# Performance work log

Measured on AMD Instinct MI355X. Metric: run time of the kernel, lower is better.

Reference implementation:

```python
import jax, jax.numpy as jnp
import numpy as np

N, D, K = 4096, 1024, 32
MARGIN = 0.3
OP_TYPE = "weighty"


def setup_inputs() -> dict:
    key = jax.random.key(0)
    k1, k2, k3, k4, k5 = jax.random.split(key, 5)
    return {
        "inputs": jax.random.normal(k1, (N, D), jnp.float32),
        "prediction": jax.random.normal(k2, (N, K), jnp.float32),
        "targets": jax.random.randint(k3, (N,), 0, K),
        "true_targets": jax.random.randint(k4, (N,), 0, K),
        "prob": jax.random.uniform(k5, (N,), jnp.float32),
        "threshold": jnp.float32(0.5),
    }


def _weighty(d1, d2, pair_type, op_type):
    # vectorized translation of weighty_new
    if op_type == "mean":
        return (d1 + d2) / 2.0
    if op_type == "max":
        return jnp.maximum(d1, d2)
    if op_type == "min":
        return jnp.minimum(d1, d2)
    if op_type == "max-min":
        return jnp.maximum(d1, d2) if pair_type == 1 else jnp.minimum(d1, d2)
    # op_type == 'weighty'
    if pair_type == 1:
        e1, e2 = jnp.exp(d1), jnp.exp(d2)
        return (e1 * d1 + e2 * d2) / (e1 + e2)
    e1, e2 = jnp.exp(-d1), jnp.exp(-d2)
    return (e1 * d1 + e2 * d2) / (e1 + e2 + 1e-6)


def reference(inputs, prediction, targets, true_targets, prob, threshold):
    n = inputs.shape[0]
    rows = jnp.arange(n)
    # pairwise euclidean dist (GEMM-based, matches addmm_ formulation)
    sq = jnp.sum(inputs * inputs, axis=1)
    dist = sq[:, None] + sq[None, :] - 2.0 * (inputs @ inputs.T)
    dist = jnp.sqrt(jnp.clip(dist, 1e-12, None))  # [n, n]

    same = targets[:, None] == targets[None, :]
    conf = prob >= threshold

    # negatives sorted ascending by dist; positives sorted descending by dist
    neg_order = jnp.argsort(jnp.where(~same, dist, jnp.inf), axis=1)   # [n,n]
    pos_order = jnp.argsort(jnp.where(same, -dist, jnp.inf), axis=1)   # [n,n]
    hp = pos_order[:, 0]   # hardest positive (max dist)
    hn = neg_order[:, 0]   # hardest negative (min dist)
    d_ap = dist[rows, hp]
    d_an = dist[rows, hn]

    cp = prob[hp] >= threshold
    cn = prob[hn] >= threshold
    fn = jnp.argmax(prediction, axis=1)[hn] == targets  # hard neg is a false negative

    # neg re-selection: ranks 1..10 first with prob>=t, else rank 11 (loop_cnt cap 10)
    neg_cand = neg_order[:, 1:12]                       # [n,11]
    ok_n = prob[neg_cand] >= threshold
    sel_n = jnp.where(ok_n[:, :10].any(axis=1), jnp.argmax(ok_n[:, :10], axis=1), 10)
    d_nn = dist[rows, neg_cand[rows, sel_n]]

    # pos re-selection: descending ranks 1..5 first with prob>=t, else rank 6 (loop_cnt cap 5)
    pos_cand = pos_order[:, 1:7]                        # [n,6]
    ok_p = prob[pos_cand] >= threshold
    sel_p = jnp.where(ok_p[:, :5].any(axis=1), jnp.argmax(ok_p[:, :5], axis=1), 5)
    d_np = dist[rows, pos_cand[rows, sel_p]]

    w1 = _weighty(d_ap, d_an, 1, OP_TYPE)
    w0 = _weighty(d_ap, d_an, 0, OP_TYPE)

    case_b = cp & (~cn) & fn                 # confident pos, unconfident FN neg
    case_cd = (~cp) & (cn | (~fn))           # unconfident pos branches that re-select pos
    inv = (~cp) & (~cn) & fn                 # inverse loss branch

    ap = jnp.where(case_b, w1, jnp.where(case_cd, d_np, d_ap))
    an = jnp.where(case_b, d_nn, jnp.where(case_cd, w0, d_an))

    per = jnp.where(inv,
                    jax.nn.relu(an - ap + MARGIN),
                    jax.nn.relu(ap - an + MARGIN))
    conff = conf.astype(per.dtype)
    cnt = jnp.sum(conf.astype(jnp.int32))
    loss = jnp.where(cnt > 0, jnp.sum(per * conff) / jnp.maximum(cnt, 1).astype(per.dtype), 0.0)
    correct = jnp.sum(((an >= ap) & conf).astype(jnp.int32))
    return loss, correct, cnt
```

## Files before the change

### kernel.cpp

```cpp
#include <hip/hip_runtime.h>
#include <hip/hip_bf16.h>
#include <stdint.h>

typedef _Float16 half8 __attribute__((ext_vector_type(8)));
typedef _Float16 half4 __attribute__((ext_vector_type(4)));
typedef float f32x4 __attribute__((ext_vector_type(4)));
typedef unsigned long long u64;

#define N_ROWS 4096
#define DIM 1024
#define KCLS 32
#define MARGIN_F 0.3f
#define SENTN 0xFFFFFFFFFFFFFFFFull

typedef const __attribute__((address_space(1))) void GASV;
typedef __attribute__((address_space(3))) void LASV;

__device__ __forceinline__ void gload_lds16(const void* g, void* l) {
    __builtin_amdgcn_global_load_lds((GASV*)g, (LASV*)l, 16, 0, 0);
}

__global__ __launch_bounds__(256) void prep_kernel(
    const float* __restrict__ inputs, const float* __restrict__ prediction,
    _Float16* __restrict__ xh, float* __restrict__ sq, int* __restrict__ pred_cls)
{
    int wid = threadIdx.x >> 6, lane = threadIdx.x & 63;
    int r = blockIdx.x * 4 + wid;
    const float* row = inputs + (size_t)r * DIM;
    _Float16* hrow = xh + (size_t)r * DIM;
    float s = 0.f;
#pragma unroll
    for (int c = 0; c < 4; ++c) {
        int idx = lane * 4 + c * 256;
        float4 v = *(const float4*)(row + idx);
        s += v.x * v.x + v.y * v.y + v.z * v.z + v.w * v.w;
        half4 h;
        h.x = (_Float16)v.x; h.y = (_Float16)v.y;
        h.z = (_Float16)v.z; h.w = (_Float16)v.w;
        *(half4*)(hrow + idx) = h;
    }
#pragma unroll
    for (int off = 32; off; off >>= 1) s += __shfl_xor(s, off);

    u64 key = 0ull;
    if (lane < KCLS) {
        unsigned b = __float_as_uint(prediction[(size_t)r * KCLS + lane]);
        unsigned u = (b & 0x80000000u) ? ~b : (b | 0x80000000u);
        key = ((u64)u << 32) | (unsigned)(KCLS - 1 - lane);
    }
#pragma unroll
    for (int off = 32; off; off >>= 1) {
        u64 o = __shfl_xor(key, off);
        if (o > key) key = o;
    }
    if (lane == 0) {
        sq[r] = s;
        pred_cls[r] = KCLS - 1 - (int)(key & 0xFFFFFFFFu);
    }
}

__global__ __launch_bounds__(512) void gemm_kernel(
    const _Float16* __restrict__ X, const float* __restrict__ sq,
    const int* __restrict__ targets,
    float* __restrict__ out, int mode, int rb0)
{
    __shared__ __align__(16) _Float16 As[128 * 64];
    __shared__ __align__(16) _Float16 Bs[128 * 64];
    int tid = threadIdx.x;

    int bx, by;
    bool diag = false, mirror = false;
    if (mode == 0) {
        int u = ((int)blockIdx.x & 7) * 66 + ((int)blockIdx.x >> 3);
        int t_ = (int)((sqrtf(8.f * u + 1.f) - 1.f) * 0.5f);
        while ((t_ + 1) * (t_ + 2) / 2 <= u) ++t_;
        while (t_ * (t_ + 1) / 2 > u) --t_;
        by = t_;
        bx = u - t_ * (t_ + 1) / 2;
        diag = (bx == by);
        mirror = !diag;
    } else {
        int nwg = gridDim.x;
        int q = nwg >> 3;
        int swz = ((int)blockIdx.x & 7) * q + ((int)blockIdx.x >> 3);
        int nbx = nwg / 32;
        bx = swz % nbx;
        by = swz / nbx;
    }

    int rs = tid >> 3;
    int ss = tid & 7;
    int srcslot = ss ^ (rs & 7);
    const _Float16* gA = X + (size_t)(rb0 + bx * 128 + rs) * DIM + srcslot * 8;
    const _Float16* gB = X + (size_t)(by * 128 + rs) * DIM + srcslot * 8;
    _Float16* lA = As + tid * 8;
    _Float16* lB = Bs + tid * 8;

    int wid = tid >> 6, lane = tid & 63;
    int wr = (wid >> 2) * 64, wc = (wid & 3) * 32;
    int fr = lane & 15, q4 = lane >> 4;

    f32x4 acc[4][2];
#pragma unroll
    for (int m = 0; m < 4; ++m)
#pragma unroll
        for (int n = 0; n < 2; ++n) acc[m][n] = (f32x4){0.f, 0.f, 0.f, 0.f};

    for (int k0 = 0; k0 < DIM; k0 += 64) {
#pragma unroll
        for (int p = 0; p < 2; ++p) {
            gload_lds16(gA + k0 + (size_t)(p * 64) * DIM, lA + p * 4096);
            if (!diag) gload_lds16(gB + k0 + (size_t)(p * 64) * DIM, lB + p * 4096);
        }
        __syncthreads();
        const _Float16* Bsrc = diag ? As : Bs;
#pragma unroll
        for (int ks = 0; ks < 2; ++ks) {
            half8 a[4], b[2];
#pragma unroll
            for (int m = 0; m < 4; ++m) {
                int row = wr + m * 16 + fr;
                int s = (ks * 4 + q4) ^ (row & 7);
                a[m] = *(const half8*)(As + row * 64 + s * 8);
            }
#pragma unroll
            for (int n = 0; n < 2; ++n) {
                int brow = wc + n * 16 + fr;
                int s = (ks * 4 + q4) ^ (brow & 7);
                b[n] = *(const half8*)(Bsrc + brow * 64 + s * 8);
            }
#pragma unroll
            for (int m = 0; m < 4; ++m)
#pragma unroll
                for (int n = 0; n < 2; ++n)
                    acc[m][n] = __builtin_amdgcn_mfma_f32_16x16x32_f16(a[m], b[n], acc[m][n], 0, 0, 0);
        }
        __syncthreads();
    }

    int rbase = rb0 + bx * 128 + wr + q4 * 4;
    float sqr_[4][4];
    int trr[4][4];
#pragma unroll
    for (int m = 0; m < 4; ++m)
#pragma unroll
        for (int q = 0; q < 4; ++q) {
            sqr_[m][q] = sq[rbase + m * 16 + q];
            trr[m][q] = targets[rbase + m * 16 + q];
        }

#pragma unroll
    for (int n = 0; n < 2; ++n) {
        int col = by * 128 + wc + n * 16 + fr;
        float sqc = sq[col];
        int tc = targets[col];
#pragma unroll
        for (int m = 0; m < 4; ++m) {
            int row0 = rbase + m * 16;
            float4 d;
            unsigned u0, u1, u2, u3;
            u0 = __float_as_uint(fmaxf(sqr_[m][0] + sqc - 2.f * acc[m][n][0], 1e-12f));
            u1 = __float_as_uint(fmaxf(sqr_[m][1] + sqc - 2.f * acc[m][n][1], 1e-12f));
            u2 = __float_as_uint(fmaxf(sqr_[m][2] + sqc - 2.f * acc[m][n][2], 1e-12f));
            u3 = __float_as_uint(fmaxf(sqr_[m][3] + sqc - 2.f * acc[m][n][3], 1e-12f));
            d.x = __uint_as_float((u0 & ~1u) | (unsigned)(trr[m][0] == tc));
            d.y = __uint_as_float((u1 & ~1u) | (unsigned)(trr[m][1] == tc));
            d.z = __uint_as_float((u2 & ~1u) | (unsigned)(trr[m][2] == tc));
            d.w = __uint_as_float((u3 & ~1u) | (unsigned)(trr[m][3] == tc));
            out[(size_t)(row0 + 0) * N_ROWS + col] = d.x;
            out[(size_t)(row0 + 1) * N_ROWS + col] = d.y;
            out[(size_t)(row0 + 2) * N_ROWS + col] = d.z;
            out[(size_t)(row0 + 3) * N_ROWS + col] = d.w;
            if (mirror)
                *(float4*)&out[(size_t)col * N_ROWS + row0] = d;
        }
    }
}

__global__ __launch_bounds__(256) void select_kernel(
    const float* __restrict__ dot,
    const int* __restrict__ targets, const float* __restrict__ prob,
    const int* __restrict__ pred_cls, const float* __restrict__ thr_p,
    int rb0, float* __restrict__ per_term, int* __restrict__ corr_flag)
{
    __shared__ unsigned Tn[4], Tp[4];
    __shared__ u64 negCand[64];
    __shared__ u64 posCand[64];
    __shared__ unsigned cnts[2];
    __shared__ u64 sN[12], sP[7];
    __shared__ u64 red[4];
    __shared__ u64 bcast;

    int t = threadIdx.x, lane = t & 63, w = t >> 6;
    int rloc = blockIdx.x, r = rb0 + rloc;
    const float* drow = dot + (size_t)rloc * N_ROWS;

    if (t < 64) { negCand[t] = SENTN; posCand[t] = 0ull; }
    if (t < 2) cnts[t] = 0u;

    unsigned bits[16];
    unsigned mneg = 0xFFFFFFFFu, mpos = 0u;
#pragma unroll
    for (int q = 0; q < 4; ++q) {
        int col0 = q * 1024 + t * 4;
        float4 dv = *(const float4*)(drow + col0);
        int j = q * 4;
        unsigned b;
        b = __float_as_uint(dv.x); bits[j + 0] = b;
        if (b & 1u) mpos = mpos > b ? mpos : b; else mneg = mneg < b ? mneg : b;
        b = __float_as_uint(dv.y); bits[j + 1] = b;
        if (b & 1u) mpos = mpos > b ? mpos : b; else mneg = mneg < b ? mneg : b;
        b = __float_as_uint(dv.z); bits[j + 2] = b;
        if (b & 1u) mpos = mpos > b ? mpos : b; else mneg = mneg < b ? mneg : b;
        b = __float_as_uint(dv.w); bits[j + 3] = b;
        if (b & 1u) mpos = mpos > b ? mpos : b; else mneg = mneg < b ? mneg : b;
    }

    unsigned T3 = 0xFFFFFFFFu, m = mneg;
#pragma unroll
    for (int rd = 0; rd < 3; ++rd) {
        unsigned b = m;
#pragma unroll
        for (int off = 32; off; off >>= 1) {
            unsigned o = __shfl_xor(b, off);
            b = o < b ? o : b;
        }
        T3 = b;
        if (m == b) m = 0xFFFFFFFFu;
    }
    unsigned P2 = 0u, mp = mpos;
#pragma unroll
    for (int rd = 0; rd < 2; ++rd) {
        unsigned b = mp;
#pragma unroll
        for (int off = 32; off; off >>= 1) {
            unsigned o = __shfl_xor(b, off);
            b = o > b ? o : b;
        }
        P2 = b;
        if (mp == b) mp = 0u;
    }
    if (lane == 0) { Tn[w] = T3; Tp[w] = P2; }
    __syncthreads();

    unsigned TnB = Tn[0];
    TnB = Tn[1] > TnB ? Tn[1] : TnB;
    TnB = Tn[2] > TnB ? Tn[2] : TnB;
    TnB = Tn[3] > TnB ? Tn[3] : TnB;
    unsigned TpB = Tp[0];
    TpB = Tp[1] < TpB ? Tp[1] : TpB;
    TpB = Tp[2] < TpB ? Tp[2] : TpB;
    TpB = Tp[3] < TpB ? Tp[3] : TpB;

#pragma unroll
    for (int q = 0; q < 4; ++q) {
#pragma unroll
        for (int e = 0; e < 4; ++e) {
            int j = q * 4 + e;
            int col = q * 1024 + t * 4 + e;
            unsigned b = bits[j];
            if (!(b & 1u) && b <= TnB) {
                unsigned s = atomicAdd(&cnts[0], 1u);
                if (s < 64u) negCand[s] = ((u64)b << 32) | (unsigned)col;
            }
            if ((b & 1u) && b >= TpB) {
                unsigned s = atomicAdd(&cnts[1], 1u);
                if (s < 64u) posCand[s] = ((u64)b << 32) | (unsigned)(N_ROWS - 1 - col);
            }
        }
    }
    __syncthreads();

    bool fb = (cnts[0] > 64u) || (cnts[1] > 64u);

    if (!fb) {
        if (w == 0) {
            u64 v = negCand[lane];
#pragma unroll
            for (int k = 2; k <= 64; k <<= 1) {
#pragma unroll
                for (int j = 32; j; j >>= 1) {
                    if (j >= k) continue;
                    u64 o = __shfl_xor(v, j);
                    bool up = (lane & k) == 0;
                    bool small = (lane & j) == 0;
                    bool keepmin = (small == up);
                    u64 lo = v < o ? v : o, hi = v < o ? o : v;
                    v = keepmin ? lo : hi;
                }
            }
            if (lane < 12) sN[lane] = v;
        } else if (w == 1) {
            u64 v = ~posCand[lane];
#pragma unroll
            for (int k = 2; k <= 64; k <<= 1) {
#pragma unroll
                for (int j = 32; j; j >>= 1) {
                    if (j >= k) continue;
                    u64 o = __shfl_xor(v, j);
                    bool up = (lane & k) == 0;
                    bool small = (lane & j) == 0;
                    bool keepmin = (small == up);
                    u64 lo = v < o ? v : o, hi = v < o ? o : v;
                    v = keepmin ? lo : hi;
                }
            }
            if (lane < 7) sP[lane] = ~v;
        }
    } else {
        unsigned remN = 0, remP = 0;
        for (int rd = 0; rd < 12; ++rd) {
            u64 best = SENTN;
#pragma unroll
            for (int q = 0; q < 4; ++q)
#pragma unroll
                for (int e = 0; e < 4; ++e) {
                    int j = q * 4 + e;
                    int col = q * 1024 + t * 4 + e;
                    bool valid = !(bits[j] & 1u) && !((remN >> j) & 1u);
                    u64 nk = valid ? (((u64)bits[j] << 32) | (unsigned)col) : SENTN;
                    best = nk < best ? nk : best;
                }
#pragma unroll
            for (int off = 32; off; off >>= 1) {
                u64 o = __shfl_xor(best, off);
                best = o < best ? o : best;
            }
            if (lane == 0) red[w] = best;
            __syncthreads();
            if (t == 0) {
                u64 b0 = red[0];
                b0 = red[1] < b0 ? red[1] : b0;
                b0 = red[2] < b0 ? red[2] : b0;
                b0 = red[3] < b0 ? red[3] : b0;
                sN[rd] = b0; bcast = b0;
            }
            __syncthreads();
            u64 b0 = bcast;
#pragma unroll
            for (int q = 0; q < 4; ++q)
#pragma unroll
                for (int e = 0; e < 4; ++e) {
                    int j = q * 4 + e;
                    int col = q * 1024 + t * 4 + e;
                    if ((((u64)bits[j] << 32) | (unsigned)col) == b0) remN |= 1u << j;
                }
            __syncthreads();
        }
        for (int rd = 0; rd < 7; ++rd) {
            u64 best = 0ull;
#pragma unroll
            for (int q = 0; q < 4; ++q)
#pragma unroll
                for (int e = 0; e < 4; ++e) {
                    int j = q * 4 + e;
                    int col = q * 1024 + t * 4 + e;
                    bool valid = (bits[j] & 1u) && !((remP >> j) & 1u);
                    u64 pk = valid ? (((u64)bits[j] << 32) | (unsigned)(N_ROWS - 1 - col)) : 0ull;
                    best = pk > best ? pk : best;
                }
#pragma unroll
            for (int off = 32; off; off >>= 1) {
                u64 o = __shfl_xor(best, off);
                best = o > best ? o : best;
            }
            if (lane == 0) red[w] = best;
            __syncthreads();
            if (t == 0) {
                u64 b0 = red[0];
                b0 = red[1] > b0 ? red[1] : b0;
                b0 = red[2] > b0 ? red[2] : b0;
                b0 = red[3] > b0 ? red[3] : b0;
                sP[rd] = b0; bcast = b0;
            }
            __syncthreads();
            u64 b0 = bcast;
#pragma unroll
            for (int q = 0; q < 4; ++q)
#pragma unroll
                for (int e = 0; e < 4; ++e) {
                    int j = q * 4 + e;
                    int col = q * 1024 + t * 4 + e;
                    if ((((u64)bits[j] << 32) | (unsigned)(N_ROWS - 1 - col)) == b0) remP |= 1u << j;
                }
            __syncthreads();
        }
    }
    __syncthreads();

    if (w == 0) {
        float thr = *thr_p;
        int tr = targets[r];
        u64 kN = (lane < 12) ? sN[lane] : SENTN;
        u64 kP = (lane >= 32 && lane < 39) ? sP[lane - 32] : 0ull;
        int idxN = ((int)(kN & 0xFFFFFFFFull)) & (N_ROWS - 1);
        int idxP = (N_ROWS - 1 - (int)(kP & 0xFFFFFFFFull)) & (N_ROWS - 1);
        bool confN = (lane < 12) && kN != SENTN && (prob[idxN] >= thr);
        bool confP = (lane >= 32 && lane < 39) && kP != 0ull && (prob[idxP] >= thr);
        u64 balN = __ballot(confN);
        u64 balP = __ballot(confP);

        u64 mN_ = balN & 0x7FEull;
        int selN = mN_ ? (__ffsll(mN_) - 1) : 11;
        unsigned dnn_bits = __shfl((unsigned)(kN >> 32), selN);
        u64 mP_ = balP & (0x3Eull << 32);
        int selP = mP_ ? (__ffsll(mP_) - 1) : 38;
        unsigned dnp_bits = __shfl((unsigned)(kP >> 32), selP);
        unsigned dap_bits = __shfl((unsigned)(kP >> 32), 32);

        if (lane == 0) {
            float d_ap = sqrtf(__uint_as_float(dap_bits));
            float d_an = sqrtf(__uint_as_float((unsigned)(kN >> 32)));
            int hn = idxN;
            bool cp = (balP >> 32) & 1ull;
            bool cn = balN & 1ull;
            bool fn = (pred_cls[hn] == tr);
            float d_nn = sqrtf(__uint_as_float(dnn_bits));
            float d_np = sqrtf(__uint_as_float(dnp_bits));

            float e1p = __expf(d_ap), e2p = __expf(d_an);
            float w1 = (e1p * d_ap + e2p * d_an) / (e1p + e2p);
            float e1n = __expf(-d_ap), e2n = __expf(-d_an);
            float w0 = (e1n * d_ap + e2n * d_an) / (e1n + e2n + 1e-6f);
            bool case_b = cp && !cn && fn;
            bool case_cd = !cp && (cn || !fn);
            bool inv = !cp && !cn && fn;
            float ap = case_b ? w1 : (case_cd ? d_np : d_ap);
            float an = case_b ? d_nn : (case_cd ? w0 : d_an);
            float per = inv ? fmaxf(an - ap + MARGIN_F, 0.f)
                            : fmaxf(ap - an + MARGIN_F, 0.f);
            per_term[r] = per;
            corr_flag[r] = (an >= ap) ? 1 : 0;
        }
    }
}

__global__ __launch_bounds__(256) void finalize_kernel(
    const float* __restrict__ per_term, const int* __restrict__ corr_flag,
    const float* __restrict__ prob, const float* __restrict__ thr_p,
    float* __restrict__ out)
{
    __shared__ float sred[4]; __shared__ int cred[4]; __shared__ int nred[4];
    float thr = *thr_p;
    int t = threadIdx.x, lane = t & 63, wid = t >> 6;
    float s = 0.f; int c = 0, n = 0;
    for (int i = t; i < N_ROWS; i += 256) {
        if (prob[i] >= thr) {
            s += per_term[i];
            c += corr_flag[i];
            n += 1;
        }
    }
#pragma unroll
    for (int off = 32; off; off >>= 1) {
        s += __shfl_xor(s, off);
        c += __shfl_xor(c, off);
        n += __shfl_xor(n, off);
    }
    if (lane == 0) { sred[wid] = s; cred[wid] = c; nred[wid] = n; }
    __syncthreads();
    if (t == 0) {
        float ss = sred[0] + sred[1] + sred[2] + sred[3];
        int cc = cred[0] + cred[1] + cred[2] + cred[3];
        int nn = nred[0] + nred[1] + nred[2] + nred[3];
        float loss = (nn > 0) ? ss / (float)nn : 0.f;
        out[0] = loss;
        out[1] = (float)cc;
        out[2] = (float)nn;
    }
}

extern "C" void kernel_launch(void* const* d_in, const int* in_sizes, int n_in,
                              void* d_out, int out_size, void* d_ws, size_t ws_size,
                              hipStream_t stream)
{
    const float* inputs     = (const float*)d_in[0];
    const float* prediction = (const float*)d_in[1];
    const int*   targets    = (const int*)d_in[2];
    const float* prob       = (const float*)d_in[4];
    const float* thr        = (const float*)d_in[5];
    float* out = (float*)d_out;

    char* ws = (char*)d_ws;
    size_t off = 0;
    auto alloc = [&](size_t bytes) -> char* {
        char* p = ws + off;
        off = (off + bytes + 255) & ~(size_t)255;
        return p;
    };
    _Float16* xh     = (_Float16*)alloc((size_t)N_ROWS * DIM * sizeof(_Float16));
    float* sq        = (float*)alloc((size_t)N_ROWS * 4);
    int*   pred_cls  = (int*)alloc((size_t)N_ROWS * 4);
    float* per_term  = (float*)alloc((size_t)N_ROWS * 4);
    int*   corr_flag = (int*)alloc((size_t)N_ROWS * 4);

    size_t avail = (ws_size > off) ? (ws_size - off) : 0;
    size_t rowbytes = (size_t)N_ROWS * 4;
    int RB = 128;
    while (RB * 2 <= N_ROWS && (size_t)(RB * 2) * rowbytes <= avail) RB *= 2;
    float* dotbuf = (float*)alloc((size_t)RB * rowbytes);

    hipLaunchKernelGGL(prep_kernel, dim3(N_ROWS / 4), dim3(256), 0, stream,
                       inputs, prediction, xh, sq, pred_cls);
    if (RB == N_ROWS) {
        hipLaunchKernelGGL(gemm_kernel, dim3(528), dim3(512), 0, stream,
                           xh, sq, targets, dotbuf, 0, 0);
        hipLaunchKernelGGL(select_kernel, dim3(N_ROWS), dim3(256), 0, stream,
                           dotbuf, targets, prob, pred_cls, thr, 0,
                           per_term, corr_flag);
    } else {
        for (int rb0 = 0; rb0 < N_ROWS; rb0 += RB) {
            hipLaunchKernelGGL(gemm_kernel, dim3((RB / 128) * 32), dim3(512), 0, stream,
                               xh, sq, targets, dotbuf, 1, rb0);
            hipLaunchKernelGGL(select_kernel, dim3(RB), dim3(256), 0, stream,
                               dotbuf, targets, prob, pred_cls, thr, rb0,
                               per_term, corr_flag);
        }
    }
    hipLaunchKernelGGL(finalize_kernel, dim3(1), dim3(256), 0, stream,
                       per_term, corr_flag, prob, thr, out);
}
```

Baseline: 83.53 us.

## Store squared distances as fp16 with same-class flag to halve intermediate traffic

The GEMM epilogue now writes each squared distance as an fp16 value, with the sign bit carrying the same-class flag, instead of a 32-bit float with the flag in the low bit. The selection kernel reads 16-bit entries and packs value and column into 32-bit sort keys instead of 64-bit keys, so its shuffles, bitonic sorts and shared-memory use get cheaper. This halves the write and read traffic of the 4096x4096 intermediate matrix. The risk is fp16 precision: squared distances near 2048 keep only about 11 bits, so ties and ordering errors among the closest or farthest candidates can change which samples are chosen and shift the loss.

```diff
diff --git a/kernel.cpp b/kernel.cpp
--- a/kernel.cpp
+++ b/kernel.cpp
@@ -5,13 +5,14 @@
 typedef _Float16 half8 __attribute__((ext_vector_type(8)));
 typedef _Float16 half4 __attribute__((ext_vector_type(4)));
 typedef float f32x4 __attribute__((ext_vector_type(4)));
+typedef unsigned short ushort8v __attribute__((ext_vector_type(8)));
+typedef unsigned short ushort4v __attribute__((ext_vector_type(4)));
 typedef unsigned long long u64;
 
 #define N_ROWS 4096
 #define DIM 1024
 #define KCLS 32
 #define MARGIN_F 0.3f
-#define SENTN 0xFFFFFFFFFFFFFFFFull
 
 typedef const __attribute__((address_space(1))) void GASV;
 typedef __attribute__((address_space(3))) void LASV;
@@ -62,7 +63,7 @@
 __global__ __launch_bounds__(512) void gemm_kernel(
     const _Float16* __restrict__ X, const float* __restrict__ sq,
     const int* __restrict__ targets,
-    float* __restrict__ out, int mode, int rb0)
+    unsigned short* __restrict__ out, int mode, int rb0)
 {
     __shared__ __align__(16) _Float16 As[128 * 64];
     __shared__ __align__(16) _Float16 Bs[128 * 64];
@@ -157,63 +158,58 @@
 #pragma unroll
         for (int m = 0; m < 4; ++m) {
             int row0 = rbase + m * 16;
-            float4 d;
-            unsigned u0, u1, u2, u3;
-            u0 = __float_as_uint(fmaxf(sqr_[m][0] + sqc - 2.f * acc[m][n][0], 1e-12f));
-            u1 = __float_as_uint(fmaxf(sqr_[m][1] + sqc - 2.f * acc[m][n][1], 1e-12f));
-            u2 = __float_as_uint(fmaxf(sqr_[m][2] + sqc - 2.f * acc[m][n][2], 1e-12f));
-            u3 = __float_as_uint(fmaxf(sqr_[m][3] + sqc - 2.f * acc[m][n][3], 1e-12f));
-            d.x = __uint_as_float((u0 & ~1u) | (unsigned)(trr[m][0] == tc));
-            d.y = __uint_as_float((u1 & ~1u) | (unsigned)(trr[m][1] == tc));
-            d.z = __uint_as_float((u2 & ~1u) | (unsigned)(trr[m][2] == tc));
-            d.w = __uint_as_float((u3 & ~1u) | (unsigned)(trr[m][3] == tc));
-            out[(size_t)(row0 + 0) * N_ROWS + col] = d.x;
-            out[(size_t)(row0 + 1) * N_ROWS + col] = d.y;
-            out[(size_t)(row0 + 2) * N_ROWS + col] = d.z;
-            out[(size_t)(row0 + 3) * N_ROWS + col] = d.w;
+            ushort4v hv;
+#pragma unroll
+            for (int q = 0; q < 4; ++q) {
+                float d2v = fmaxf(sqr_[m][q] + sqc - 2.f * acc[m][n][q], 1e-12f);
+                _Float16 h = (_Float16)d2v;
+                unsigned short hb = __builtin_bit_cast(unsigned short, h);
+                hb = (unsigned short)(hb | ((trr[m][q] == tc) ? 0x8000u : 0u));
+                hv[q] = hb;
+                out[(size_t)(row0 + q) * N_ROWS + col] = hb;
+            }
             if (mirror)
-                *(float4*)&out[(size_t)col * N_ROWS + row0] = d;
+                *(ushort4v*)&out[(size_t)col * N_ROWS + row0] = hv;
         }
     }
 }
 
 __global__ __launch_bounds__(256) void select_kernel(
-    const float* __restrict__ dot,
+    const unsigned short* __restrict__ dot,
     const int* __restrict__ targets, const float* __restrict__ prob,
     const int* __restrict__ pred_cls, const float* __restrict__ thr_p,
     int rb0, float* __restrict__ per_term, int* __restrict__ corr_flag)
 {
     __shared__ unsigned Tn[4], Tp[4];
-    __shared__ u64 negCand[64];
-    __shared__ u64 posCand[64];
+    __shared__ unsigned negCand[64];
+    __shared__ unsigned posCand[64];
     __shared__ unsigned cnts[2];
-    __shared__ u64 sN[12], sP[7];
-    __shared__ u64 red[4];
-    __shared__ u64 bcast;
+    __shared__ unsigned sN[12], sP[7];
+    __shared__ unsigned red[4];
+    __shared__ unsigned bcast;
 
     int t = threadIdx.x, lane = t & 63, w = t >> 6;
     int rloc = blockIdx.x, r = rb0 + rloc;
-    const float* drow = dot + (size_t)rloc * N_ROWS;
-
-    if (t < 64) { negCand[t] = SENTN; posCand[t] = 0ull; }
+    const unsigned short* drow = dot + (size_t)rloc * N_ROWS;
+
+    if (t < 64) { negCand[t] = 0xFFFFFFFFu; posCand[t] = 0u; }
     if (t < 2) cnts[t] = 0u;
 
-    unsigned bits[16];
+    unsigned short hb[16];
     unsigned mneg = 0xFFFFFFFFu, mpos = 0u;
-#pragma unroll
-    for (int q = 0; q < 4; ++q) {
-        int col0 = q * 1024 + t * 4;
-        float4 dv = *(const float4*)(drow + col0);
-        int j = q * 4;
-        unsigned b;
-        b = __float_as_uint(dv.x); bits[j + 0] = b;
-        if (b & 1u) mpos = mpos > b ? mpos : b; else mneg = mneg < b ? mneg : b;
-        b = __float_as_uint(dv.y); bits[j + 1] = b;
-        if (b & 1u) mpos = mpos > b ? mpos : b; else mneg = mneg < b ? mneg : b;
-        b = __float_as_uint(dv.z); bits[j + 2] = b;
-        if (b & 1u) mpos = mpos > b ? mpos : b; else mneg = mneg < b ? mneg : b;
-        b = __float_as_uint(dv.w); bits[j + 3] = b;
-        if (b & 1u) mpos = mpos > b ? mpos : b; else mneg = mneg < b ? mneg : b;
+    {
+        ushort8v v0 = *(const ushort8v*)(drow + t * 8);
+        ushort8v v1 = *(const ushort8v*)(drow + 2048 + t * 8);
+#pragma unroll
+        for (int j = 0; j < 8; ++j) {
+            unsigned b = v0[j]; hb[j] = (unsigned short)b;
+            if (b & 0x8000u) mpos = mpos > b ? mpos : b; else mneg = mneg < b ? mneg : b;
+        }
+#pragma unroll
+        for (int j = 0; j < 8; ++j) {
+            unsigned b = v1[j]; hb[8 + j] = (unsigned short)b;
+            if (b & 0x8000u) mpos = mpos > b ? mpos : b; else mneg = mneg < b ? mneg : b;
+        }
     }
 
     unsigned T3 = 0xFFFFFFFFu, m = mneg;
@@ -253,20 +249,16 @@
     TpB = Tp[3] < TpB ? Tp[3] : TpB;
 
 #pragma unroll
-    for (int q = 0; q < 4; ++q) {
-#pragma unroll
-        for (int e = 0; e < 4; ++e) {
-            int j = q * 4 + e;
-            int col = q * 1024 + t * 4 + e;
-            unsigned b = bits[j];
-            if (!(b & 1u) && b <= TnB) {
-                unsigned s = atomicAdd(&cnts[0], 1u);
-                if (s < 64u) negCand[s] = ((u64)b << 32) | (unsigned)col;
-            }
-            if ((b & 1u) && b >= TpB) {
-                unsigned s = atomicAdd(&cnts[1], 1u);
-                if (s < 64u) posCand[s] = ((u64)b << 32) | (unsigned)(N_ROWS - 1 - col);
-            }
+    for (int j = 0; j < 16; ++j) {
+        int col = (j < 8) ? (t * 8 + j) : (2048 + t * 8 + (j - 8));
+        unsigned b = hb[j];
+        if (!(b & 0x8000u) && b <= TnB) {
+            unsigned s = atomicAdd(&cnts[0], 1u);
+            if (s < 64u) negCand[s] = (b << 16) | (unsigned)col;
+        }
+        if ((b & 0x8000u) && b >= TpB) {
+            unsigned s = atomicAdd(&cnts[1], 1u);
+            if (s < 64u) posCand[s] = (b << 16) | (unsigned)(N_ROWS - 1 - col);
         }
     }
     __syncthreads();
@@ -275,33 +267,33 @@
 
     if (!fb) {
         if (w == 0) {
-            u64 v = negCand[lane];
+            unsigned v = negCand[lane];
 #pragma unroll
             for (int k = 2; k <= 64; k <<= 1) {
 #pragma unroll
                 for (int j = 32; j; j >>= 1) {
                     if (j >= k) continue;
-                    u64 o = __shfl_xor(v, j);
+                    unsigned o = __shfl_xor(v, j);
                     bool up = (lane & k) == 0;
                     bool small = (lane & j) == 0;
                     bool keepmin = (small == up);
-                    u64 lo = v < o ? v : o, hi = v < o ? o : v;
+                    unsigned lo = v < o ? v : o, hi = v < o ? o : v;
                     v = keepmin ? lo : hi;
                 }
             }
             if (lane < 12) sN[lane] = v;
         } else if (w == 1) {
-            u64 v = ~posCand[lane];
+            unsigned v = ~posCand[lane];
 #pragma unroll
             for (int k = 2; k <= 64; k <<= 1) {
 #pragma unroll
                 for (int j = 32; j; j >>= 1) {
                     if (j >= k) continue;
-                    u64 o = __shfl_xor(v, j);
+                    unsigned o = __shfl_xor(v, j);
                     bool up = (lane & k) == 0;
                     bool small = (lane & j) == 0;
                     bool keepmin = (small == up);
-                    u64 lo = v < o ? v : o, hi = v < o ? o : v;
+                    unsigned lo = v < o ? v : o, hi = v < o ? o : v;
                     v = keepmin ? lo : hi;
                 }
             }
@@ -310,79 +302,69 @@
     } else {
         unsigned remN = 0, remP = 0;
         for (int rd = 0; rd < 12; ++rd) {
-            u64 best = SENTN;
-#pragma unroll
-            for (int q = 0; q < 4; ++q)
-#pragma unroll
-                for (int e = 0; e < 4; ++e) {
-                    int j = q * 4 + e;
-                    int col = q * 1024 + t * 4 + e;
-                    bool valid = !(bits[j] & 1u) && !((remN >> j) & 1u);
-                    u64 nk = valid ? (((u64)bits[j] << 32) | (unsigned)col) : SENTN;
-                    best = nk < best ? nk : best;
-                }
+            unsigned best = 0xFFFFFFFFu;
+#pragma unroll
+            for (int j = 0; j < 16; ++j) {
+                int col = (j < 8) ? (t * 8 + j) : (2048 + t * 8 + (j - 8));
+                unsigned b = hb[j];
+                bool valid = !(b & 0x8000u) && !((remN >> j) & 1u);
+                unsigned nk = valid ? ((b << 16) | (unsigned)col) : 0xFFFFFFFFu;
+                best = nk < best ? nk : best;
+            }
 #pragma unroll
             for (int off = 32; off; off >>= 1) {
-                u64 o = __shfl_xor(best, off);
+                unsigned o = __shfl_xor(best, off);
                 best = o < best ? o : best;
             }
             if (lane == 0) red[w] = best;
             __syncthreads();
             if (t == 0) {
-                u64 b0 = red[0];
+                unsigned b0 = red[0];
                 b0 = red[1] < b0 ? red[1] : b0;
                 b0 = red[2] < b0 ? red[2] : b0;
                 b0 = red[3] < b0 ? red[3] : b0;
                 sN[rd] = b0; bcast = b0;
             }
             __syncthreads();
-            u64 b0 = bcast;
-#pragma unroll
-            for (int q = 0; q < 4; ++q)
-#pragma unroll
-                for (int e = 0; e < 4; ++e) {
-                    int j = q * 4 + e;
-                    int col = q * 1024 + t * 4 + e;
-                    if ((((u64)bits[j] << 32) | (unsigned)col) == b0) remN |= 1u << j;
-                }
+            unsigned b0 = bcast;
+#pragma unroll
+            for (int j = 0; j < 16; ++j) {
+                int col = (j < 8) ? (t * 8 + j) : (2048 + t * 8 + (j - 8));
+                if ((((unsigned)hb[j] << 16) | (unsigned)col) == b0) remN |= 1u << j;
+            }
             __syncthreads();
         }
         for (int rd = 0; rd < 7; ++rd) {
-            u64 best = 0ull;
-#pragma unroll
-            for (int q = 0; q < 4; ++q)
-#pragma unroll
-                for (int e = 0; e < 4; ++e) {
-                    int j = q * 4 + e;
-                    int col = q * 1024 + t * 4 + e;
-                    bool valid = (bits[j] & 1u) && !((remP >> j) & 1u);
-                    u64 pk = valid ? (((u64)bits[j] << 32) | (unsigned)(N_ROWS - 1 - col)) : 0ull;
-                    best = pk > best ? pk : best;
-                }
+            unsigned best = 0u;
+#pragma unroll
+            for (int j = 0; j < 16; ++j) {
+                int col = (j < 8) ? (t * 8 + j) : (2048 + t * 8 + (j - 8));
+                unsigned b = hb[j];
+                bool valid = (b & 0x8000u) && !((remP >> j) & 1u);
+                unsigned pk = valid ? ((b << 16) | (unsigned)(N_ROWS - 1 - col)) : 0u;
+                best = pk > best ? pk : best;
+            }
 #pragma unroll
             for (int off = 32; off; off >>= 1) {
-                u64 o = __shfl_xor(best, off);
+                unsigned o = __shfl_xor(best, off);
                 best = o > best ? o : best;
             }
             if (lane == 0) red[w] = best;
             __syncthreads();
             if (t == 0) {
-                u64 b0 = red[0];
+                unsigned b0 = red[0];
                 b0 = red[1] > b0 ? red[1] : b0;
                 b0 = red[2] > b0 ? red[2] : b0;
                 b0 = red[3] > b0 ? red[3] : b0;
                 sP[rd] = b0; bcast = b0;
             }
             __syncthreads();
-            u64 b0 = bcast;
-#pragma unroll
-            for (int q = 0; q < 4; ++q)
-#pragma unroll
-                for (int e = 0; e < 4; ++e) {
-                    int j = q * 4 + e;
-                    int col = q * 1024 + t * 4 + e;
-                    if ((((u64)bits[j] << 32) | (unsigned)(N_ROWS - 1 - col)) == b0) remP |= 1u << j;
-                }
+            unsigned b0 = bcast;
+#pragma unroll
+            for (int j = 0; j < 16; ++j) {
+                int col = (j < 8) ? (t * 8 + j) : (2048 + t * 8 + (j - 8));
+                if ((((unsigned)hb[j] << 16) | (unsigned)(N_ROWS - 1 - col)) == b0) remP |= 1u << j;
+            }
             __syncthreads();
         }
     }
@@ -391,32 +373,37 @@
     if (w == 0) {
         float thr = *thr_p;
         int tr = targets[r];
-        u64 kN = (lane < 12) ? sN[lane] : SENTN;
-        u64 kP = (lane >= 32 && lane < 39) ? sP[lane - 32] : 0ull;
-        int idxN = ((int)(kN & 0xFFFFFFFFull)) & (N_ROWS - 1);
-        int idxP = (N_ROWS - 1 - (int)(kP & 0xFFFFFFFFull)) & (N_ROWS - 1);
-        bool confN = (lane < 12) && kN != SENTN && (prob[idxN] >= thr);
-        bool confP = (lane >= 32 && lane < 39) && kP != 0ull && (prob[idxP] >= thr);
+        unsigned kN = (lane < 12) ? sN[lane] : 0xFFFFFFFFu;
+        unsigned kP = (lane >= 32 && lane < 39) ? sP[lane - 32] : 0u;
+        int idxN = (int)(kN & 0xFFFFu) & (N_ROWS - 1);
+        int idxP = (N_ROWS - 1 - (int)(kP & 0xFFFFu)) & (N_ROWS - 1);
+        bool confN = (lane < 12) && kN != 0xFFFFFFFFu && (prob[idxN] >= thr);
+        bool confP = (lane >= 32 && lane < 39) && kP != 0u && (prob[idxP] >= thr);
         u64 balN = __ballot(confN);
         u64 balP = __ballot(confP);
 
         u64 mN_ = balN & 0x7FEull;
         int selN = mN_ ? (__ffsll(mN_) - 1) : 11;
-        unsigned dnn_bits = __shfl((unsigned)(kN >> 32), selN);
+        unsigned dnn_b = __shfl(kN >> 16, selN);
         u64 mP_ = balP & (0x3Eull << 32);
         int selP = mP_ ? (__ffsll(mP_) - 1) : 38;
-        unsigned dnp_bits = __shfl((unsigned)(kP >> 32), selP);
-        unsigned dap_bits = __shfl((unsigned)(kP >> 32), 32);
+        unsigned dnp_b = __shfl(kP >> 16, selP);
+        unsigned dap_b = __shfl(kP >> 16, 32);
 
         if (lane == 0) {
-            float d_ap = sqrtf(__uint_as_float(dap_bits));
-            float d_an = sqrtf(__uint_as_float((unsigned)(kN >> 32)));
+            auto h2f = [](unsigned b16) -> float {
+                unsigned short us = (unsigned short)(b16 & 0x7FFFu);
+                _Float16 h = __builtin_bit_cast(_Float16, us);
+                return (float)h;
+            };
+            float d_ap = sqrtf(h2f(dap_b));
+            float d_an = sqrtf(h2f(kN >> 16));
             int hn = idxN;
             bool cp = (balP >> 32) & 1ull;
             bool cn = balN & 1ull;
             bool fn = (pred_cls[hn] == tr);
-            float d_nn = sqrtf(__uint_as_float(dnn_bits));
-            float d_np = sqrtf(__uint_as_float(dnp_bits));
+            float d_nn = sqrtf(h2f(dnn_b));
+            float d_np = sqrtf(h2f(dnp_b));
 
             float e1p = __expf(d_ap), e2p = __expf(d_an);
             float w1 = (e1p * d_ap + e2p * d_an) / (e1p + e2p);
@@ -495,10 +482,10 @@
     int*   corr_flag = (int*)alloc((size_t)N_ROWS * 4);
 
     size_t avail = (ws_size > off) ? (ws_size - off) : 0;
-    size_t rowbytes = (size_t)N_ROWS * 4;
+    size_t rowbytes = (size_t)N_ROWS * 2;
     int RB = 128;
     while (RB * 2 <= N_ROWS && (size_t)(RB * 2) * rowbytes <= avail) RB *= 2;
-    float* dotbuf = (float*)alloc((size_t)RB * rowbytes);
+    unsigned short* dotbuf = (unsigned short*)alloc((size_t)RB * rowbytes);
 
     hipLaunchKernelGGL(prep_kernel, dim3(N_ROWS / 4), dim3(256), 0, stream,
                        inputs, prediction, xh, sq, pred_cls);
```

After: 76.15 us. 1.1x faster.
